# Optimization experiments

Measured on AMD Instinct MI355X. Metric: run time of the kernel, lower is better.

The kernel has to match this reference:

```python
import jax, jax.numpy as jnp
import numpy as np

# dims / config (from init_kwargs)
B, N, D, H = 8, 512, 256, 8
M, K, R = 8, 16, 8            # n_slots basis graphs, slot_dim, kernel_rank
DH = D // H
SCALE = 1.0 / float(np.sqrt(D))
TAU_AFF, TAU_SLOT = 1.0, 1.0
GW_EPS, GW_SIGMA = 0.05, 1.0
GW_OUTER, GW_SINK, TOL = 3, 10, 1e-6
G_DIV_LAMBDA, USAGE_LAMBDA, EPS = 0.1, 0.01, 1e-8


def setup_inputs() -> dict:
    key = jax.random.key(0)
    ks = jax.random.split(key, 9)
    xav = lambda k, shp: jax.random.normal(k, shp, jnp.float32) * float(np.sqrt(2.0 / (shp[-2] + shp[-1])))
    return {
        "x_desc": jax.random.normal(ks[0], (B, N, D), jnp.float32),
        "x_name": jax.random.normal(ks[1], (B, N, D), jnp.float32),
        "W1": xav(ks[2], (2 * D, D)), "b1": jnp.zeros((D,), jnp.float32),
        "W2": xav(ks[3], (D, D)),     "b2": jnp.zeros((D,), jnp.float32),
        "Wp": xav(ks[4], (D, M)),     "bp": jnp.zeros((M,), jnp.float32),
        "U_param": xav(ks[5], (M, K, R)),
    }


def _forward(x_desc, x_name, W1, b1, W2, b2, Wp, bp, U_param):
    # fusion MLP: Linear -> ReLU -> Linear
    z = jnp.concatenate([x_desc, x_name], axis=-1)          # [B,N,2D]
    z = jax.nn.relu(z @ W1 + b1) @ W2 + b2                  # [B,N,D]

    # per-head l2-normalized affinity, no self loop
    zh = z.reshape(B, N, H, DH).transpose(0, 2, 1, 3)       # [B,H,N,DH]
    zh = zh / jnp.clip(jnp.linalg.norm(zh, axis=-1, keepdims=True), 1e-8)
    logits = jnp.einsum('bhnd,bhsd->bhns', zh, zh) * (SCALE / TAU_AFF)
    logits = jnp.where(jnp.eye(N, dtype=bool), -1e9, logits)
    P = jax.nn.softmax(logits, axis=-1)                     # [B,H,N,N]

    # normalize_affinity (symmetrize + row-stochastic) -> distance
    Pn = 0.5 * (P + P.swapaxes(-1, -2))
    Pn = jnp.clip(Pn, EPS)
    Pn = Pn / jnp.clip(Pn.sum(-1, keepdims=True), EPS)
    DP = jnp.clip(1.0 - Pn, 0.0)                            # [B,H,N,N]

    # slot graphs G = softplus(U) softplus(U)^T, row-stochastic (kernel_row_stoch)
    U = jax.nn.softplus(U_param)                            # [M,K,R]
    G = jnp.einsum('mkr,mjr->mkj', U, U)                    # [M,K,K]
    G = G / jnp.clip(G.sum(-1, keepdims=True), EPS)

    # Frobenius diversity reg across the M graphs
    V = G.reshape(M, -1)
    V = V / jnp.clip(jnp.linalg.norm(V, axis=1, keepdims=True), 1e-8)
    Gram = V @ V.T
    g_reg = G_DIV_LAMBDA * (Gram.sum() - jnp.trace(Gram)) / (M * (M - 1))

    # cosine slot cost -> DG [M,K,K], zero diagonal
    diag = jnp.clip(jnp.diagonal(G, axis1=-2, axis2=-1), EPS)      # [M,K]
    denom = jnp.clip(jnp.sqrt(diag[:, :, None] * diag[:, None, :]), EPS)
    DG = jnp.clip(1.0 - jnp.clip(G / denom, -1.0, 1.0), 0.0)
    DG = DG * (1.0 - jnp.eye(K, dtype=DG.dtype))

    # entropic Gromov-Wasserstein between DP (nodes) and each DG_m (slots),
    # vectorized over the M graphs. a uniform over N, b uniform over K.
    Dx2, Dy2 = DP ** 2, DG ** 2
    a_w, b_w = 1.0 / N, 1.0 / K
    Pi = jnp.full((B, H, M, N, K), a_w * b_w, jnp.float32)

    def sinkhorn(C):
        Kmat = jnp.clip(jnp.exp(-C / GW_EPS), 1e-12)
        def body(i, uv):
            u, v = uv
            u = a_w / (jnp.einsum('bhmnk,bhmk->bhmn', Kmat, v) + TOL)
            v = b_w / (jnp.einsum('bhmnk,bhmn->bhmk', Kmat, u) + TOL)
            return (u, v)
        u0 = jnp.full((B, H, M, N), 1.0 / N, jnp.float32)
        v0 = jnp.full((B, H, M, K), 1.0 / K, jnp.float32)
        u, v = jax.lax.fori_loop(0, GW_SINK, body, (u0, v0))
        return u[..., :, None] * Kmat * v[..., None, :]

    C = None
    for _ in range(GW_OUTER):
        mass_j = Pi.sum(-1)                                  # [B,H,M,N]
        mass_l = Pi.sum(-2)                                  # [B,H,M,K]
        term1 = jnp.einsum('bhij,bhmj->bhmi', Dx2, mass_j)[..., :, None]
        term2 = jnp.einsum('mkl,bhml->bhmk', Dy2, mass_l)[..., None, :]
        cross = jnp.einsum('bhij,bhmjl,mkl->bhmik', DP, Pi, DG)
        C = jnp.clip(term1 + term2 - 2.0 * cross, 0.0)       # [B,H,M,N,K]
        Pi = sinkhorn(C)
    gw_val = (C * Pi).sum((-2, -1))                          # [B,H,M]

    # alpha weights over M graphs (alpha_from_gw)
    scores = jnp.exp(-(gw_val / GW_SIGMA) ** 2)
    alpha = scores / jnp.clip(scores.sum(-1, keepdims=True), 1e-8)

    # transport slot graphs back to node space, alpha-mix, row-normalize
    T = jnp.einsum('bhmnk,mkl->bhmnl', Pi, G)                # [B,H,M,N,K]
    Qmix = jnp.einsum('bhm,bhmnl,bhmsl->bhns', alpha, T, Pi)
    Qmix = jnp.clip(Qmix, EPS)
    Q = Qmix / Qmix.sum(-1, keepdims=True)                   # [B,H,N,N]
    bias_log = jnp.log(jax.lax.stop_gradient(Q))             # detached log-prior

    # slot usage regularizer (KL to uniform over M)
    A = jax.nn.softmax((z @ Wp + bp) / TAU_SLOT, axis=-1)     # [B,N,M]
    usage = A.mean((0, 1))
    usage_kl = jnp.sum(usage * jnp.log(jnp.clip(usage, EPS) * M))
    total_reg = g_reg + USAGE_LAMBDA * usage_kl
    return bias_log, Q, total_reg


def reference(x_desc, x_name, W1, b1, W2, b2, Wp, bp, U_param):
    return _forward(x_desc, x_name, W1, b1, W2, b2, Wp, bp, U_param)
```

## Files before the change

kernel.cpp:

```cpp
#include <hip/hip_runtime.h>
#include <cstdint>
#include <cstddef>

#define NB 8
#define NN 512
#define ND 256
#define NH 8
#define NM 8
#define NK 16
#define NR 8
#define NDH 32
#define BN (NB*NN)
#define BH (NB*NH)
#define BHN (BH*NN)
#define BHM (BH*NM)
#define QOFF 16777216

typedef __attribute__((ext_vector_type(8))) short bf16x8;
typedef __attribute__((ext_vector_type(8))) unsigned short u16x8;
typedef __attribute__((ext_vector_type(4))) float f32x4;

__device__ inline unsigned short f2bf(float x) {
  union { float f; unsigned u; } c; c.f = x;
  unsigned r = c.u + 0x7FFFu + ((c.u >> 16) & 1u);
  return (unsigned short)(r >> 16);
}
__device__ inline float bf2f(unsigned short x) {
  union { unsigned u; float f; } c; c.u = ((unsigned)x) << 16; return c.f;
}

__global__ __launch_bounds__(256) void k_mlp1(const float* __restrict__ xd, const float* __restrict__ xn,
                       const float* __restrict__ W1, const float* __restrict__ b1,
                       float* __restrict__ hid) {
  __shared__ float As[16][68];
  __shared__ float Bs[16][68];
  int t = threadIdx.x;
  int col0 = blockIdx.x * 64;
  int row0 = blockIdx.y * 64;
  int ar = t >> 2, ak = (t & 3) * 4;
  int bk = t >> 4, bc = (t & 15) * 4;
  int ty = t >> 4, tx = t & 15;
  float acc[4][4] = {};
  for (int k0 = 0; k0 < 2*ND; k0 += 16) {
    int gk = k0 + ak;
    const float* src = (gk < ND) ? (xd + (size_t)(row0+ar)*ND + gk)
                                 : (xn + (size_t)(row0+ar)*ND + (gk-ND));
    float4 av = *(const float4*)src;
    As[ak+0][ar] = av.x; As[ak+1][ar] = av.y; As[ak+2][ar] = av.z; As[ak+3][ar] = av.w;
    float4 bv = *(const float4*)(W1 + (size_t)(k0+bk)*ND + col0 + bc);
    *(float4*)&Bs[bk][bc] = bv;
    __syncthreads();
    #pragma unroll
    for (int kk = 0; kk < 16; kk++) {
      float4 a = *(const float4*)&As[kk][ty*4];
      float4 b = *(const float4*)&Bs[kk][tx*4];
      acc[0][0] += a.x*b.x; acc[0][1] += a.x*b.y; acc[0][2] += a.x*b.z; acc[0][3] += a.x*b.w;
      acc[1][0] += a.y*b.x; acc[1][1] += a.y*b.y; acc[1][2] += a.y*b.z; acc[1][3] += a.y*b.w;
      acc[2][0] += a.z*b.x; acc[2][1] += a.z*b.y; acc[2][2] += a.z*b.z; acc[2][3] += a.z*b.w;
      acc[3][0] += a.w*b.x; acc[3][1] += a.w*b.y; acc[3][2] += a.w*b.z; acc[3][3] += a.w*b.w;
    }
    __syncthreads();
  }
  float4 bb = *(const float4*)(b1 + col0 + tx*4);
  #pragma unroll
  for (int a = 0; a < 4; a++) {
    float4 o;
    o.x = fmaxf(acc[a][0] + bb.x, 0.f);
    o.y = fmaxf(acc[a][1] + bb.y, 0.f);
    o.z = fmaxf(acc[a][2] + bb.z, 0.f);
    o.w = fmaxf(acc[a][3] + bb.w, 0.f);
    *(float4*)(hid + (size_t)(row0+ty*4+a)*ND + col0 + tx*4) = o;
  }
}

__global__ __launch_bounds__(256) void k_mlp2(const float* __restrict__ hidp,
                       const float* __restrict__ W2, const float* __restrict__ b2,
                       float* __restrict__ z) {
  __shared__ float As[16][68];
  __shared__ float Bs[16][68];
  int t = threadIdx.x;
  int col0 = blockIdx.x * 64;
  int row0 = blockIdx.y * 64;
  int ar = t >> 2, ak = (t & 3) * 4;
  int bk = t >> 4, bc = (t & 15) * 4;
  int ty = t >> 4, tx = t & 15;
  float acc[4][4] = {};
  for (int k0 = 0; k0 < ND; k0 += 16) {
    float4 av = *(const float4*)(hidp + (size_t)(row0+ar)*ND + k0 + ak);
    As[ak+0][ar] = av.x; As[ak+1][ar] = av.y; As[ak+2][ar] = av.z; As[ak+3][ar] = av.w;
    float4 bv = *(const float4*)(W2 + (size_t)(k0+bk)*ND + col0 + bc);
    *(float4*)&Bs[bk][bc] = bv;
    __syncthreads();
    #pragma unroll
    for (int kk = 0; kk < 16; kk++) {
      float4 a = *(const float4*)&As[kk][ty*4];
      float4 b = *(const float4*)&Bs[kk][tx*4];
      acc[0][0] += a.x*b.x; acc[0][1] += a.x*b.y; acc[0][2] += a.x*b.z; acc[0][3] += a.x*b.w;
      acc[1][0] += a.y*b.x; acc[1][1] += a.y*b.y; acc[1][2] += a.y*b.z; acc[1][3] += a.y*b.w;
      acc[2][0] += a.z*b.x; acc[2][1] += a.z*b.y; acc[2][2] += a.z*b.z; acc[2][3] += a.z*b.w;
      acc[3][0] += a.w*b.x; acc[3][1] += a.w*b.y; acc[3][2] += a.w*b.z; acc[3][3] += a.w*b.w;
    }
    __syncthreads();
  }
  float4 bb = *(const float4*)(b2 + col0 + tx*4);
  #pragma unroll
  for (int a = 0; a < 4; a++) {
    float4 o;
    o.x = acc[a][0] + bb.x; o.y = acc[a][1] + bb.y;
    o.z = acc[a][2] + bb.z; o.w = acc[a][3] + bb.w;
    *(float4*)(z + (size_t)(row0+ty*4+a)*ND + col0 + tx*4) = o;
  }
}

__global__ void k_zhnorm(const float* __restrict__ z, float* __restrict__ zh) {
  int idx = blockIdx.x*256 + threadIdx.x;
  int d = idx & 31;
  int n = (idx >> 5) & (NN-1);
  int h = (idx >> 14) & (NH-1);
  int b = idx >> 17;
  float v = z[(size_t)(b*NN + n)*ND + h*NDH + d];
  float ss = v*v;
  #pragma unroll
  for (int m = 1; m < 32; m <<= 1) ss += __shfl_xor(ss, m);
  zh[idx] = v / fmaxf(sqrtf(ss), 1e-8f);
}

__global__ __launch_bounds__(256) void k_affinity(const float* __restrict__ zh, unsigned short* __restrict__ P) {
  int blk = blockIdx.x;
  int rt = blk & 15, bh = blk >> 4;
  int r0 = rt*32;
  const float* base = zh + (size_t)bh*NN*NDH;
  __shared__ float qs[32][33];
  __shared__ float ks[32][36];
  int t = threadIdx.x;
  int sr = t >> 3, dq = (t & 7)*4;
  {
    float4 v = *(const float4*)(base + (size_t)(r0+sr)*NDH + dq);
    qs[sr][dq] = v.x; qs[sr][dq+1] = v.y; qs[sr][dq+2] = v.z; qs[sr][dq+3] = v.w;
  }
  int cr = t >> 3;
  int cq = t & 7;
  float acc[16][4];
  #pragma unroll
  for (int ti = 0; ti < 16; ti++) { acc[ti][0]=0; acc[ti][1]=0; acc[ti][2]=0; acc[ti][3]=0; }
  for (int ti = 0; ti < 16; ti++) {
    int s0 = ti*32;
    __syncthreads();
    {
      float4 v = *(const float4*)(base + (size_t)(s0+sr)*NDH + dq);
      ks[dq+0][sr] = v.x; ks[dq+1][sr] = v.y; ks[dq+2][sr] = v.z; ks[dq+3][sr] = v.w;
    }
    __syncthreads();
    #pragma unroll
    for (int d = 0; d < 32; d++) {
      float qv = qs[cr][d];
      float4 kv = *(const float4*)&ks[d][cq*4];
      acc[ti][0] += qv*kv.x; acc[ti][1] += qv*kv.y;
      acc[ti][2] += qv*kv.z; acc[ti][3] += qv*kv.w;
    }
  }
  int gr = r0 + cr;
  float mx = -1e30f;
  #pragma unroll
  for (int ti = 0; ti < 16; ti++) {
    #pragma unroll
    for (int j = 0; j < 4; j++) {
      int s = ti*32 + cq*4 + j;
      float v = (s == gr) ? -1e9f : acc[ti][j]*0.0625f;
      acc[ti][j] = v;
      mx = fmaxf(mx, v);
    }
  }
  mx = fmaxf(mx, __shfl_xor(mx, 1));
  mx = fmaxf(mx, __shfl_xor(mx, 2));
  mx = fmaxf(mx, __shfl_xor(mx, 4));
  float sum = 0.f;
  #pragma unroll
  for (int ti = 0; ti < 16; ti++) {
    #pragma unroll
    for (int j = 0; j < 4; j++) { float e = expf(acc[ti][j]-mx); acc[ti][j] = e; sum += e; }
  }
  sum += __shfl_xor(sum,1); sum += __shfl_xor(sum,2); sum += __shfl_xor(sum,4);
  float inv = 1.f/sum;
  unsigned short* prow = P + ((size_t)(bh*NN) + gr)*NN;
  #pragma unroll
  for (int ti = 0; ti < 16; ti++) {
    uint2 pk;
    pk.x = (unsigned)f2bf(acc[ti][0]*inv) | ((unsigned)f2bf(acc[ti][1]*inv) << 16);
    pk.y = (unsigned)f2bf(acc[ti][2]*inv) | ((unsigned)f2bf(acc[ti][3]*inv) << 16);
    *(uint2*)(prow + ti*32 + cq*4) = pk;
  }
}

__global__ __launch_bounds__(256) void k_dp(const unsigned short* __restrict__ P,
                       unsigned short* __restrict__ DPo, unsigned short* __restrict__ DPq) {
  int blk = blockIdx.x;
  int rt = blk & 15, bh = blk >> 4;
  int r0 = rt*32;
  const unsigned short* Pb = P + (size_t)bh*NN*NN;
  __shared__ float Bs[32][33];
  int t = threadIdx.x;
  int r = t >> 3, q4 = (t & 7)*4;
  float pn[16][4];
  float rowacc = 0.f;
  for (int ti = 0; ti < 16; ti++) {
    int s0 = ti*32;
    __syncthreads();
    {
      uint2 v = *(const uint2*)(Pb + (size_t)(s0+r)*NN + r0 + q4);
      Bs[r][q4+0] = bf2f((unsigned short)(v.x & 0xFFFF));
      Bs[r][q4+1] = bf2f((unsigned short)(v.x >> 16));
      Bs[r][q4+2] = bf2f((unsigned short)(v.y & 0xFFFF));
      Bs[r][q4+3] = bf2f((unsigned short)(v.y >> 16));
    }
    uint2 av = *(const uint2*)(Pb + (size_t)(r0+r)*NN + s0 + q4);
    __syncthreads();
    float a0 = bf2f((unsigned short)(av.x & 0xFFFF));
    float a1 = bf2f((unsigned short)(av.x >> 16));
    float a2 = bf2f((unsigned short)(av.y & 0xFFFF));
    float a3 = bf2f((unsigned short)(av.y >> 16));
    float p0 = fmaxf(0.5f*(a0 + Bs[q4+0][r]), 1e-8f);
    float p1 = fmaxf(0.5f*(a1 + Bs[q4+1][r]), 1e-8f);
    float p2 = fmaxf(0.5f*(a2 + Bs[q4+2][r]), 1e-8f);
    float p3 = fmaxf(0.5f*(a3 + Bs[q4+3][r]), 1e-8f);
    pn[ti][0]=p0; pn[ti][1]=p1; pn[ti][2]=p2; pn[ti][3]=p3;
    rowacc += p0+p1+p2+p3;
  }
  rowacc += __shfl_xor(rowacc,1); rowacc += __shfl_xor(rowacc,2); rowacc += __shfl_xor(rowacc,4);
  float inv = 1.f / fmaxf(rowacc, 1e-8f);
  unsigned short* drow = DPo + ((size_t)(bh*NN) + r0 + r)*NN;
  unsigned short* qrow = DPq + ((size_t)(bh*NN) + r0 + r)*NN;
  #pragma unroll
  for (int ti = 0; ti < 16; ti++) {
    float o0 = fmaxf(1.f - pn[ti][0]*inv, 0.f);
    float o1 = fmaxf(1.f - pn[ti][1]*inv, 0.f);
    float o2 = fmaxf(1.f - pn[ti][2]*inv, 0.f);
    float o3 = fmaxf(1.f - pn[ti][3]*inv, 0.f);
    uint2 pk;
    pk.x = (unsigned)f2bf(o0) | ((unsigned)f2bf(o1) << 16);
    pk.y = (unsigned)f2bf(o2) | ((unsigned)f2bf(o3) << 16);
    *(uint2*)(drow + ti*32 + q4) = pk;
    uint2 qk;
    qk.x = (unsigned)f2bf(o0*o0) | ((unsigned)f2bf(o1*o1) << 16);
    qk.y = (unsigned)f2bf(o2*o2) | ((unsigned)f2bf(o3*o3) << 16);
    *(uint2*)(qrow + ti*32 + q4) = qk;
  }
}

__global__ void k_slots(const float* __restrict__ Up, float* __restrict__ G,
                        float* __restrict__ DG, float* __restrict__ greg) {
  __shared__ float U[NM*NK*NR];
  __shared__ float Gs[NM*NK*NK];
  __shared__ float rs[NM*NK];
  __shared__ float vn[NM];
  __shared__ float gram[NM*NM];
  int t = threadIdx.x;
  for (int i = t; i < NM*NK*NR; i += 256) {
    float x = Up[i];
    U[i] = fmaxf(x, 0.f) + log1pf(expf(-fabsf(x)));
  }
  __syncthreads();
  for (int i = t; i < NM*NK*NK; i += 256) {
    int m = i >> 8, k = (i >> 4) & 15, j = i & 15;
    float acc = 0.f;
    #pragma unroll
    for (int r = 0; r < NR; r++) acc += U[(m*NK+k)*NR + r]*U[(m*NK+j)*NR + r];
    Gs[i] = acc;
  }
  __syncthreads();
  for (int i = t; i < NM*NK; i += 256) {
    float s = 0.f;
    #pragma unroll
    for (int j = 0; j < NK; j++) s += Gs[i*NK + j];
    rs[i] = fmaxf(s, 1e-8f);
  }
  __syncthreads();
  for (int i = t; i < NM*NK*NK; i += 256) { Gs[i] /= rs[i >> 4]; G[i] = Gs[i]; }
  __syncthreads();
  for (int i = t; i < NM; i += 256) {
    float s = 0.f;
    for (int j = 0; j < NK*NK; j++) { float g = Gs[i*NK*NK + j]; s += g*g; }
    vn[i] = fmaxf(sqrtf(s), 1e-8f);
  }
  __syncthreads();
  for (int i = t; i < NM*NM; i += 256) {
    int a = i >> 3, b = i & 7;
    float s = 0.f;
    for (int j = 0; j < NK*NK; j++) s += Gs[a*NK*NK + j]*Gs[b*NK*NK + j];
    gram[i] = s / (vn[a]*vn[b]);
  }
  __syncthreads();
  if (t == 0) {
    float s = 0.f;
    for (int i = 0; i < NM*NM; i++) if ((i >> 3) != (i & 7)) s += gram[i];
    greg[0] = 0.1f * s / (float)(NM*(NM-1));
  }
  for (int i = t; i < NM*NK*NK; i += 256) {
    int m = i >> 8, k = (i >> 4) & 15, j = i & 15;
    float dk = fmaxf(Gs[m*NK*NK + k*NK + k], 1e-8f);
    float dj = fmaxf(Gs[m*NK*NK + j*NK + j], 1e-8f);
    float den = fmaxf(sqrtf(dk*dj), 1e-8f);
    float c = fminf(fmaxf(Gs[i]/den, -1.f), 1.f);
    float d = fmaxf(1.f - c, 0.f);
    if (k == j) d = 0.f;
    DG[i] = d;
  }
}

#define KSTR 513
#define PSTR 520
__global__ __launch_bounds__(512, 4) void k_gw(
    const unsigned short* __restrict__ DPb,
    const unsigned short* __restrict__ DPq,
    const float* __restrict__ Gm,
    const float* __restrict__ DGm,
    unsigned short* __restrict__ PiGs,
    unsigned short* __restrict__ Pis,
    float* __restrict__ gwv) {
  int blk = blockIdx.x;
  int xcd = blk & 7, seq = blk >> 3;
  int bh = xcd*8 + (seq >> 3);
  int m  = seq & 7;
  __shared__ float KT[16*KSTR];
  __shared__ unsigned short PiT[16*PSTR];
  __shared__ float u[512];
  __shared__ float vv[16], ml[16], t2s[16];
  __shared__ float Gs[16][17], DGs[16][17];
  __shared__ float sred[8][16];
  int t = threadIdx.x;
  int lane = t & 63, w = t >> 6;
  int il = lane & 15, q = lane >> 4;
  if (t < 256) { Gs[t>>4][t&15] = Gm[m*256 + t]; DGs[t>>4][t&15] = DGm[m*256 + t]; }
  for (int i = t; i < 16*PSTR; i += 512) PiT[i] = 0x3900;
  const unsigned short* DPbase = DPb + (size_t)bh*NN*NN;
  const unsigned short* DQbase = DPq + (size_t)bh*NN*NN;
  float creg[4][4];
  float gwp = 0.f;
  int rbase = w*64;
  __syncthreads();
  for (int it = 0; it < 3; ++it) {
    if (t < 16) {
      float s = 0.f;
      #pragma unroll
      for (int l = 0; l < 16; l++) { float d = DGs[t][l]; s += d*d*((it == 0) ? (1.f/16.f) : ml[l]); }
      t2s[t] = s;
    }
    __syncthreads();
    f32x4 aW0={0,0,0,0}, aW1={0,0,0,0}, aW2={0,0,0,0}, aW3={0,0,0,0};
    f32x4 aV0={0,0,0,0}, aV1={0,0,0,0}, aV2={0,0,0,0}, aV3={0,0,0,0};
    #pragma unroll 2
    for (int jt = 0; jt < 16; jt++) {
      bf16x8 af = *(const bf16x8*)&PiT[il*PSTR + jt*32 + q*8];
      const unsigned short* pr = DPbase + (size_t)(rbase + il)*NN + jt*32 + q*8;
      const unsigned short* qr = DQbase + (size_t)(rbase + il)*NN + jt*32 + q*8;
      bf16x8 w0 = *(const bf16x8*)(pr);
      bf16x8 w1 = *(const bf16x8*)(pr + 16*NN);
      bf16x8 w2 = *(const bf16x8*)(pr + 32*NN);
      bf16x8 w3 = *(const bf16x8*)(pr + 48*NN);
      bf16x8 v0 = *(const bf16x8*)(qr);
      bf16x8 v1 = *(const bf16x8*)(qr + 16*NN);
      bf16x8 v2 = *(const bf16x8*)(qr + 32*NN);
      bf16x8 v3 = *(const bf16x8*)(qr + 48*NN);
      aW0 = __builtin_amdgcn_mfma_f32_16x16x32_bf16(af, w0, aW0, 0, 0, 0);
      aW1 = __builtin_amdgcn_mfma_f32_16x16x32_bf16(af, w1, aW1, 0, 0, 0);
      aW2 = __builtin_amdgcn_mfma_f32_16x16x32_bf16(af, w2, aW2, 0, 0, 0);
      aW3 = __builtin_amdgcn_mfma_f32_16x16x32_bf16(af, w3, aW3, 0, 0, 0);
      aV0 = __builtin_amdgcn_mfma_f32_16x16x32_bf16(af, v0, aV0, 0, 0, 0);
      aV1 = __builtin_amdgcn_mfma_f32_16x16x32_bf16(af, v1, aV1, 0, 0, 0);
      aV2 = __builtin_amdgcn_mfma_f32_16x16x32_bf16(af, v2, aV2, 0, 0, 0);
      aV3 = __builtin_amdgcn_mfma_f32_16x16x32_bf16(af, v3, aV3, 0, 0, 0);
    }
    #pragma unroll
    for (int tt = 0; tt < 4; tt++) {
      f32x4 av = (tt==0)?aW0:((tt==1)?aW1:((tt==2)?aW2:aW3));
      f32x4 bv = (tt==0)?aV0:((tt==1)?aV1:((tt==2)?aV2:aV3));
      float tv = bv[0]+bv[1]+bv[2]+bv[3];
      tv += __shfl_xor(tv, 16); tv += __shfl_xor(tv, 32);
      float pc[16];
      #pragma unroll
      for (int k = 0; k < 16; k++) {
        pc[k] = av[0]*DGs[k][q*4+0] + av[1]*DGs[k][q*4+1]
              + av[2]*DGs[k][q*4+2] + av[3]*DGs[k][q*4+3];
      }
      #pragma unroll
      for (int k = 0; k < 16; k++) { pc[k] += __shfl_xor(pc[k], 16); pc[k] += __shfl_xor(pc[k], 32); }
      int i = rbase + tt*16 + il;
      #pragma unroll
      for (int kk = 0; kk < 4; kk++) {
        int k = q*4 + kk;
        float c = fmaxf(tv + t2s[k] - 2.f*pc[k], 0.f);
        creg[tt][kk] = c;
        KT[k*KSTR + i] = fmaxf(__expf(-20.f*c), 1e-12f);
      }
    }
    __syncthreads();
    if (t < 16) vv[t] = 1.f/16.f;
    __syncthreads();
    for (int si = 0; si < 10; si++) {
      float s = 0.f;
      #pragma unroll
      for (int k = 0; k < 16; k++) s += KT[k*KSTR + t]*vv[k];
      u[t] = (1.f/512.f)/(s + 1e-6f);
      __syncthreads();
      {
        int g = t >> 4, k = t & 15;
        float p = 0.f;
        #pragma unroll
        for (int jj = 0; jj < 16; jj++) { int j = g*16 + jj; p += KT[k*KSTR + j]*u[j]; }
        p += __shfl_xor(p, 16); p += __shfl_xor(p, 32);
        if (lane < 16) sred[w][lane] = p;
      }
      __syncthreads();
      if (t < 16) {
        float S = 0.f;
        #pragma unroll
        for (int w2 = 0; w2 < 8; w2++) S += sred[w2][t];
        vv[t] = (1.f/16.f)/(S + 1e-6f);
      }
      __syncthreads();
    }
    if (it < 2) {
      {
        int g = t >> 4, k = t & 15;
        float p = 0.f;
        #pragma unroll
        for (int jj = 0; jj < 16; jj++) { int j = g*16 + jj; p += KT[k*KSTR + j]*u[j]; }
        p += __shfl_xor(p, 16); p += __shfl_xor(p, 32);
        if (lane < 16) sred[w][lane] = p;
      }
      __syncthreads();
      if (t < 16) {
        float S = 0.f;
        #pragma unroll
        for (int w2 = 0; w2 < 8; w2++) S += sred[w2][t];
        ml[t] = vv[t]*S;
      }
      {
        int g = t >> 4, k = t & 15;
        float vk = vv[k];
        #pragma unroll
        for (int qq = 0; qq < 8; qq++) {
          int j0 = g*16 + qq*2;
          float p0 = u[j0]*KT[k*KSTR + j0]*vk;
          float p1 = u[j0+1]*KT[k*KSTR + j0+1]*vk;
          unsigned pk = (unsigned)f2bf(p0) | ((unsigned)f2bf(p1) << 16);
          *(unsigned*)&PiT[k*PSTR + j0] = pk;
        }
      }
      __syncthreads();
    } else {
      float pi[16];
      #pragma unroll
      for (int k = 0; k < 16; k++) pi[k] = u[t]*KT[k*KSTR + t]*vv[k];
      size_t ob = ((size_t)bh*NN + t)*128 + m*16;
      {
        uint4 w0, w1;
        w0.x = (unsigned)f2bf(pi[0])  | ((unsigned)f2bf(pi[1])  << 16);
        w0.y = (unsigned)f2bf(pi[2])  | ((unsigned)f2bf(pi[3])  << 16);
        w0.z = (unsigned)f2bf(pi[4])  | ((unsigned)f2bf(pi[5])  << 16);
        w0.w = (unsigned)f2bf(pi[6])  | ((unsigned)f2bf(pi[7])  << 16);
        w1.x = (unsigned)f2bf(pi[8])  | ((unsigned)f2bf(pi[9])  << 16);
        w1.y = (unsigned)f2bf(pi[10]) | ((unsigned)f2bf(pi[11]) << 16);
        w1.z = (unsigned)f2bf(pi[12]) | ((unsigned)f2bf(pi[13]) << 16);
        w1.w = (unsigned)f2bf(pi[14]) | ((unsigned)f2bf(pi[15]) << 16);
        *(uint4*)(Pis + ob) = w0;
        *(uint4*)(Pis + ob + 8) = w1;
      }
      float pig[16];
      #pragma unroll
      for (int l = 0; l < 16; l++) {
        float s = 0.f;
        #pragma unroll
        for (int k = 0; k < 16; k++) s += pi[k]*Gs[k][l];
        pig[l] = s;
      }
      {
        uint4 w0, w1;
        w0.x = (unsigned)f2bf(pig[0])  | ((unsigned)f2bf(pig[1])  << 16);
        w0.y = (unsigned)f2bf(pig[2])  | ((unsigned)f2bf(pig[3])  << 16);
        w0.z = (unsigned)f2bf(pig[4])  | ((unsigned)f2bf(pig[5])  << 16);
        w0.w = (unsigned)f2bf(pig[6])  | ((unsigned)f2bf(pig[7])  << 16);
        w1.x = (unsigned)f2bf(pig[8])  | ((unsigned)f2bf(pig[9])  << 16);
        w1.y = (unsigned)f2bf(pig[10]) | ((unsigned)f2bf(pig[11]) << 16);
        w1.z = (unsigned)f2bf(pig[12]) | ((unsigned)f2bf(pig[13]) << 16);
        w1.w = (unsigned)f2bf(pig[14]) | ((unsigned)f2bf(pig[15]) << 16);
        *(uint4*)(PiGs + ob) = w0;
        *(uint4*)(PiGs + ob + 8) = w1;
      }
      #pragma unroll
      for (int tt = 0; tt < 4; tt++) {
        int i = rbase + tt*16 + il;
        #pragma unroll
        for (int kk = 0; kk < 4; kk++) {
          int k = q*4 + kk;
          gwp += creg[tt][kk]*(u[i]*KT[k*KSTR + i]*vv[k]);
        }
      }
      #pragma unroll
      for (int off = 1; off < 64; off <<= 1) gwp += __shfl_xor(gwp, off);
      if (lane == 0) sred[w][0] = gwp;
      __syncthreads();
      if (t == 0) {
        float S = 0.f;
        #pragma unroll
        for (int w2 = 0; w2 < 8; w2++) S += sred[w2][0];
        gwv[bh*8 + m] = S;
      }
    }
  }
}

__global__ void k_alpha(const float* __restrict__ gw, float* __restrict__ alpha) {
  int t = threadIdx.x;
  float g = gw[t];
  float sc = expf(-(g*g));
  float s = sc;
  s += __shfl_xor(s, 1); s += __shfl_xor(s, 2); s += __shfl_xor(s, 4);
  alpha[t] = sc / fmaxf(s, 1e-8f);
}

__global__ __launch_bounds__(256) void k_qgemm(const unsigned short* __restrict__ PiGs,
                       const unsigned short* __restrict__ Pis, const float* __restrict__ alpha,
                       float* __restrict__ out) {
  int bid = blockIdx.x;
  int blk = (bid & 7)*128 + (bid >> 3);
  int strip = blk & 15, bh = blk >> 4;
  int i0 = strip*32;
  __shared__ unsigned short As[32*128];
  __shared__ unsigned short Bs[128*128];
  __shared__ float rsum[4][32];
  __shared__ float als[8];
  int t = threadIdx.x;
  int w = t >> 6, lane = t & 63;
  if (t < 8) als[t] = alpha[bh*8 + t];
  __syncthreads();
  const unsigned short* Ab = PiGs + ((size_t)bh*NN + i0)*128;
  #pragma unroll
  for (int q = 0; q < 2; q++) {
    int idx = q*256 + t;
    int r = idx >> 4, sg = idx & 15;
    float4 v = *(const float4*)(Ab + r*128 + sg*8);
    u16x8 hv = *(u16x8*)&v;
    float a = als[sg >> 1];
    u16x8 o;
    #pragma unroll
    for (int e = 0; e < 8; e++) o[e] = f2bf(bf2f(hv[e])*a);
    *(u16x8*)&As[r*128 + (sg ^ (r & 7))*8] = o;
  }
  f32x4 acc[4][2][2] = {};
  const unsigned short* Bb = Pis + (size_t)bh*NN*128;
  for (int c = 0; c < 4; c++) {
    __syncthreads();
    #pragma unroll
    for (int q = 0; q < 8; q++) {
      int idx = q*256 + t;
      int r = idx >> 4, sg = idx & 15;
      float4 v = *(const float4*)(Bb + (size_t)(c*128 + r)*128 + sg*8);
      *(float4*)&Bs[r*128 + (sg ^ (r & 7))*8] = v;
    }
    __syncthreads();
    int col0 = w*32;
    #pragma unroll
    for (int ks = 0; ks < 4; ks++) {
      int slot = (ks*4 + (lane >> 4)) ^ (lane & 7);
      int la = lane & 15;
      bf16x8 a0 = *(bf16x8*)&As[la*128 + slot*8];
      bf16x8 a1 = *(bf16x8*)&As[(la+16)*128 + slot*8];
      bf16x8 b0 = *(bf16x8*)&Bs[(col0+la)*128 + slot*8];
      bf16x8 b1 = *(bf16x8*)&Bs[(col0+la+16)*128 + slot*8];
      acc[c][0][0] = __builtin_amdgcn_mfma_f32_16x16x32_bf16(a0, b0, acc[c][0][0], 0, 0, 0);
      acc[c][1][0] = __builtin_amdgcn_mfma_f32_16x16x32_bf16(a1, b0, acc[c][1][0], 0, 0, 0);
      acc[c][0][1] = __builtin_amdgcn_mfma_f32_16x16x32_bf16(a0, b1, acc[c][0][1], 0, 0, 0);
      acc[c][1][1] = __builtin_amdgcn_mfma_f32_16x16x32_bf16(a1, b1, acc[c][1][1], 0, 0, 0);
    }
  }
  float part[2][4];
  #pragma unroll
  for (int mt = 0; mt < 2; mt++) {
    #pragma unroll
    for (int rg = 0; rg < 4; rg++) {
      float s = 0.f;
      #pragma unroll
      for (int c = 0; c < 4; c++) {
        #pragma unroll
        for (int nt = 0; nt < 2; nt++) s += fmaxf(acc[c][mt][nt][rg], 1e-8f);
      }
      s += __shfl_xor(s, 1); s += __shfl_xor(s, 2);
      s += __shfl_xor(s, 4); s += __shfl_xor(s, 8);
      part[mt][rg] = s;
    }
  }
  if ((lane & 15) == 0) {
    int rgrp = lane >> 4;
    #pragma unroll
    for (int mt = 0; mt < 2; mt++)
      #pragma unroll
      for (int rg = 0; rg < 4; rg++)
        rsum[w][mt*16 + rgrp*4 + rg] = part[mt][rg];
  }
  __syncthreads();
  float invr[2][4];
  #pragma unroll
  for (int mt = 0; mt < 2; mt++) {
    #pragma unroll
    for (int rg = 0; rg < 4; rg++) {
      int row = mt*16 + (lane >> 4)*4 + rg;
      invr[mt][rg] = 1.f / (rsum[0][row] + rsum[1][row] + rsum[2][row] + rsum[3][row]);
    }
  }
  float* Qb = out + (size_t)QOFF + ((size_t)bh*NN + i0)*NN;
  float* Lb = out + ((size_t)bh*NN + i0)*NN;
  #pragma unroll
  for (int c = 0; c < 4; c++) {
    #pragma unroll
    for (int mt = 0; mt < 2; mt++) {
      #pragma unroll
      for (int nt = 0; nt < 2; nt++) {
        #pragma unroll
        for (int rg = 0; rg < 4; rg++) {
          int row = mt*16 + (lane >> 4)*4 + rg;
          int col = c*128 + w*32 + nt*16 + (lane & 15);
          float v = fmaxf(acc[c][mt][nt][rg], 1e-8f)*invr[mt][rg];
          Qb[(size_t)row*NN + col] = v;
          Lb[(size_t)row*NN + col] = __logf(v);
        }
      }
    }
  }
}

__global__ __launch_bounds__(256) void k_usage(const float* __restrict__ z, const float* __restrict__ Wp,
                        const float* __restrict__ bp, float* __restrict__ partial) {
  __shared__ float wps[256][9];
  __shared__ float red[256][8];
  int t = threadIdx.x;
  {
    float4 a = *(const float4*)(Wp + t*8);
    float4 b = *(const float4*)(Wp + t*8 + 4);
    wps[t][0]=a.x; wps[t][1]=a.y; wps[t][2]=a.z; wps[t][3]=a.w;
    wps[t][4]=b.x; wps[t][5]=b.y; wps[t][6]=b.z; wps[t][7]=b.w;
  }
  __syncthreads();
  int row = blockIdx.x*256 + t;
  const float* zr = z + (size_t)row*ND;
  float acc[8] = {};
  for (int d0 = 0; d0 < ND; d0 += 4) {
    float4 v = *(const float4*)(zr + d0);
    #pragma unroll
    for (int m = 0; m < 8; m++) {
      acc[m] += v.x*wps[d0][m] + v.y*wps[d0+1][m] + v.z*wps[d0+2][m] + v.w*wps[d0+3][m];
    }
  }
  float mx = -1e30f;
  #pragma unroll
  for (int m = 0; m < 8; m++) { acc[m] += bp[m]; mx = fmaxf(mx, acc[m]); }
  float s = 0.f;
  #pragma unroll
  for (int m = 0; m < 8; m++) { acc[m] = expf(acc[m]-mx); s += acc[m]; }
  float inv = 1.f/s;
  #pragma unroll
  for (int m = 0; m < 8; m++) red[t][m] = acc[m]*inv;
  __syncthreads();
  for (int q = 128; q > 0; q >>= 1) {
    if (t < q) { for (int m = 0; m < 8; m++) red[t][m] += red[t+q][m]; }
    __syncthreads();
  }
  if (t < 8) partial[blockIdx.x*8 + t] = red[0][t];
}

__global__ void k_final(const float* __restrict__ greg, const float* __restrict__ partial,
                        float* __restrict__ out) {
  if (threadIdx.x == 0) {
    float us[8] = {};
    for (int b = 0; b < 16; b++)
      for (int m = 0; m < 8; m++) us[m] += partial[b*8 + m];
    float kl = 0.f;
    for (int m = 0; m < 8; m++) {
      float u = us[m] / (float)BN;
      kl += u*logf(fmaxf(u, 1e-8f)*(float)NM);
    }
    out[33554432] = greg[0] + 0.01f*kl;
  }
}

extern "C" void kernel_launch(void* const* d_in, const int* in_sizes, int n_in,
                              void* d_out, int out_size, void* d_ws, size_t ws_size,
                              hipStream_t stream) {
  const float* xd = (const float*)d_in[0];
  const float* xn = (const float*)d_in[1];
  const float* W1 = (const float*)d_in[2];
  const float* b1 = (const float*)d_in[3];
  const float* W2 = (const float*)d_in[4];
  const float* b2 = (const float*)d_in[5];
  const float* Wp = (const float*)d_in[6];
  const float* bp = (const float*)d_in[7];
  const float* Up = (const float*)d_in[8];
  float* out = (float*)d_out;
  float* ws  = (float*)d_ws;

  float* z   = ws + 0;
  float* hid = ws + 1048576;
  float* zh  = ws + 2097152;
  unsigned short* PiGs = (unsigned short*)(ws + 3145728);
  unsigned short* Pis  = (unsigned short*)(ws + 5242880);
  float* gw    = ws + 7340032;
  float* alpha = ws + 7340544;
  float* G     = ws + 7341056;
  float* DG    = ws + 7343104;
  float* greg  = ws + 7345152;
  float* partial = ws + 7345153;

  unsigned short* P16 = (unsigned short*)out;
  unsigned short* DPb = (unsigned short*)(out + QOFF);
  unsigned short* DPq = DPb + (size_t)16777216;

  k_mlp1<<<dim3(4, 64), 256, 0, stream>>>(xd, xn, W1, b1, hid);
  k_mlp2<<<dim3(4, 64), 256, 0, stream>>>(hid, W2, b2, z);
  k_usage<<<16, 256, 0, stream>>>(z, Wp, bp, partial);
  k_zhnorm<<<4096, 256, 0, stream>>>(z, zh);
  k_affinity<<<1024, 256, 0, stream>>>(zh, P16);
  k_dp<<<1024, 256, 0, stream>>>(P16, DPb, DPq);
  k_slots<<<1, 256, 0, stream>>>(Up, G, DG, greg);
  k_gw<<<512, 512, 0, stream>>>(DPb, DPq, G, DG, PiGs, Pis, gw);
  k_alpha<<<1, 512, 0, stream>>>(gw, alpha);
  k_qgemm<<<1024, 256, 0, stream>>>(PiGs, Pis, alpha, out);
  k_final<<<1, 64, 0, stream>>>(greg, partial, out);
}
```

Measured before the change: 590.1 us.

## Skip first GW cost GEMM via row sums; stage DP tiles in LDS; bf16 kernel

Row sums of DP and DP² are now produced in the DP kernel, so the first outer GW iteration, where Pi is uniform, builds the cost matrix from those sums and skips the two DP GEMMs entirely. The remaining iterations stream DP and DP² tiles through a register-prefetched LDS buffer instead of each wave reading global memory directly. The Gibbs kernel is stored in LDS as bf16 and also kept in registers. Sinkhorn marginals are folded into the last inner iteration to drop an extra reduction. This cuts global traffic and GEMM work, at the cost of more block barriers, more LDS use per block, and bf16 rounding of the kernel matrix.

```diff
diff --git a/kernel.cpp b/kernel.cpp
--- a/kernel.cpp
+++ b/kernel.cpp
@@ -27,6 +27,12 @@
 }
 __device__ inline float bf2f(unsigned short x) {
   union { unsigned u; float f; } c; c.u = ((unsigned)x) << 16; return c.f;
+}
+__device__ inline float bflo(unsigned w2) {
+  union { unsigned u; float f; } c; c.u = w2 << 16; return c.f;
+}
+__device__ inline float bfhi(unsigned w2) {
+  union { unsigned u; float f; } c; c.u = w2 & 0xFFFF0000u; return c.f;
 }
 
 __global__ __launch_bounds__(256) void k_mlp1(const float* __restrict__ xd, const float* __restrict__ xn,
@@ -193,7 +199,8 @@
 }
 
 __global__ __launch_bounds__(256) void k_dp(const unsigned short* __restrict__ P,
-                       unsigned short* __restrict__ DPo, unsigned short* __restrict__ DPq) {
+                       unsigned short* __restrict__ DPo, unsigned short* __restrict__ DPq,
+                       float* __restrict__ rs, float* __restrict__ rq) {
   int blk = blockIdx.x;
   int rt = blk & 15, bh = blk >> 4;
   int r0 = rt*32;
@@ -230,12 +237,15 @@
   float inv = 1.f / fmaxf(rowacc, 1e-8f);
   unsigned short* drow = DPo + ((size_t)(bh*NN) + r0 + r)*NN;
   unsigned short* qrow = DPq + ((size_t)(bh*NN) + r0 + r)*NN;
+  float rsv = 0.f, rqv = 0.f;
   #pragma unroll
   for (int ti = 0; ti < 16; ti++) {
     float o0 = fmaxf(1.f - pn[ti][0]*inv, 0.f);
     float o1 = fmaxf(1.f - pn[ti][1]*inv, 0.f);
     float o2 = fmaxf(1.f - pn[ti][2]*inv, 0.f);
     float o3 = fmaxf(1.f - pn[ti][3]*inv, 0.f);
+    rsv += o0+o1+o2+o3;
+    rqv += o0*o0 + o1*o1 + o2*o2 + o3*o3;
     uint2 pk;
     pk.x = (unsigned)f2bf(o0) | ((unsigned)f2bf(o1) << 16);
     pk.y = (unsigned)f2bf(o2) | ((unsigned)f2bf(o3) << 16);
@@ -245,13 +255,19 @@
     qk.y = (unsigned)f2bf(o2*o2) | ((unsigned)f2bf(o3*o3) << 16);
     *(uint2*)(qrow + ti*32 + q4) = qk;
   }
+  rsv += __shfl_xor(rsv,1); rsv += __shfl_xor(rsv,2); rsv += __shfl_xor(rsv,4);
+  rqv += __shfl_xor(rqv,1); rqv += __shfl_xor(rqv,2); rqv += __shfl_xor(rqv,4);
+  if ((t & 7) == 0) {
+    rs[bh*NN + r0 + r] = rsv;
+    rq[bh*NN + r0 + r] = rqv;
+  }
 }
 
 __global__ void k_slots(const float* __restrict__ Up, float* __restrict__ G,
                         float* __restrict__ DG, float* __restrict__ greg) {
   __shared__ float U[NM*NK*NR];
   __shared__ float Gs[NM*NK*NK];
-  __shared__ float rs[NM*NK];
+  __shared__ float rsx[NM*NK];
   __shared__ float vn[NM];
   __shared__ float gram[NM*NM];
   int t = threadIdx.x;
@@ -272,10 +288,10 @@
     float s = 0.f;
     #pragma unroll
     for (int j = 0; j < NK; j++) s += Gs[i*NK + j];
-    rs[i] = fmaxf(s, 1e-8f);
-  }
-  __syncthreads();
-  for (int i = t; i < NM*NK*NK; i += 256) { Gs[i] /= rs[i >> 4]; G[i] = Gs[i]; }
+    rsx[i] = fmaxf(s, 1e-8f);
+  }
+  __syncthreads();
+  for (int i = t; i < NM*NK*NK; i += 256) { Gs[i] /= rsx[i >> 4]; G[i] = Gs[i]; }
   __syncthreads();
   for (int i = t; i < NM; i += 256) {
     float s = 0.f;
@@ -307,151 +323,213 @@
   }
 }
 
-#define KSTR 513
+#define DSTR 40
+#define KST 522
 #define PSTR 520
 __global__ __launch_bounds__(512, 4) void k_gw(
     const unsigned short* __restrict__ DPb,
     const unsigned short* __restrict__ DPq,
-    const float* __restrict__ Gm,
-    const float* __restrict__ DGm,
-    unsigned short* __restrict__ PiGs,
-    unsigned short* __restrict__ Pis,
+    const float* __restrict__ rs, const float* __restrict__ rq,
+    const float* __restrict__ Gm, const float* __restrict__ DGm,
+    unsigned short* __restrict__ PiGs, unsigned short* __restrict__ Pis,
     float* __restrict__ gwv) {
   int blk = blockIdx.x;
   int xcd = blk & 7, seq = blk >> 3;
   int bh = xcd*8 + (seq >> 3);
   int m  = seq & 7;
-  __shared__ float KT[16*KSTR];
-  __shared__ unsigned short PiT[16*PSTR];
-  __shared__ float u[512];
-  __shared__ float vv[16], ml[16], t2s[16];
-  __shared__ float Gs[16][17], DGs[16][17];
+  __shared__ __align__(16) unsigned short DPs[512*DSTR];
+  __shared__ __align__(16) unsigned short KT[16*KST];
+  __shared__ __align__(16) unsigned short PiT[16*PSTR];
+  __shared__ __align__(16) float u[512];
+  __shared__ __align__(16) float vv[16];
+  __shared__ float ml[16], t2s[16], dgrow[16];
+  __shared__ float Gsm[16][17], DGsm[16][17];
   __shared__ float sred[8][16];
   int t = threadIdx.x;
   int lane = t & 63, w = t >> 6;
   int il = lane & 15, q = lane >> 4;
-  if (t < 256) { Gs[t>>4][t&15] = Gm[m*256 + t]; DGs[t>>4][t&15] = DGm[m*256 + t]; }
-  for (int i = t; i < 16*PSTR; i += 512) PiT[i] = 0x3900;
+  int g = t >> 4, kc = t & 15;
+  if (t < 256) { Gsm[t>>4][t&15] = Gm[m*256 + t]; DGsm[t>>4][t&15] = DGm[m*256 + t]; }
+  __syncthreads();
+  if (t < 16) {
+    float s = 0.f;
+    #pragma unroll
+    for (int l = 0; l < 16; l++) s += DGsm[t][l];
+    dgrow[t] = s;
+  }
   const unsigned short* DPbase = DPb + (size_t)bh*NN*NN;
   const unsigned short* DQbase = DPq + (size_t)bh*NN*NN;
+  float rsv = rs[bh*NN + t]*(1.f/8192.f);
+  float rqv = rq[bh*NN + t]*(1.f/512.f);
+  float Kt[16];
   float creg[4][4];
-  float gwp = 0.f;
-  int rbase = w*64;
-  __syncthreads();
-  for (int it = 0; it < 3; ++it) {
+  float ut = 0.f;
+  int r0i = t >> 2, ci = (t & 3)*8;
+  for (int itr = 0; itr < 3; ++itr) {
     if (t < 16) {
       float s = 0.f;
       #pragma unroll
-      for (int l = 0; l < 16; l++) { float d = DGs[t][l]; s += d*d*((it == 0) ? (1.f/16.f) : ml[l]); }
+      for (int l = 0; l < 16; l++) { float d = DGsm[t][l]; s += d*d*((itr == 0) ? (1.f/16.f) : ml[l]); }
       t2s[t] = s;
     }
     __syncthreads();
-    f32x4 aW0={0,0,0,0}, aW1={0,0,0,0}, aW2={0,0,0,0}, aW3={0,0,0,0};
-    f32x4 aV0={0,0,0,0}, aV1={0,0,0,0}, aV2={0,0,0,0}, aV3={0,0,0,0};
-    #pragma unroll 2
-    for (int jt = 0; jt < 16; jt++) {
-      bf16x8 af = *(const bf16x8*)&PiT[il*PSTR + jt*32 + q*8];
-      const unsigned short* pr = DPbase + (size_t)(rbase + il)*NN + jt*32 + q*8;
-      const unsigned short* qr = DQbase + (size_t)(rbase + il)*NN + jt*32 + q*8;
-      bf16x8 w0 = *(const bf16x8*)(pr);
-      bf16x8 w1 = *(const bf16x8*)(pr + 16*NN);
-      bf16x8 w2 = *(const bf16x8*)(pr + 32*NN);
-      bf16x8 w3 = *(const bf16x8*)(pr + 48*NN);
-      bf16x8 v0 = *(const bf16x8*)(qr);
-      bf16x8 v1 = *(const bf16x8*)(qr + 16*NN);
-      bf16x8 v2 = *(const bf16x8*)(qr + 32*NN);
-      bf16x8 v3 = *(const bf16x8*)(qr + 48*NN);
-      aW0 = __builtin_amdgcn_mfma_f32_16x16x32_bf16(af, w0, aW0, 0, 0, 0);
-      aW1 = __builtin_amdgcn_mfma_f32_16x16x32_bf16(af, w1, aW1, 0, 0, 0);
-      aW2 = __builtin_amdgcn_mfma_f32_16x16x32_bf16(af, w2, aW2, 0, 0, 0);
-      aW3 = __builtin_amdgcn_mfma_f32_16x16x32_bf16(af, w3, aW3, 0, 0, 0);
-      aV0 = __builtin_amdgcn_mfma_f32_16x16x32_bf16(af, v0, aV0, 0, 0, 0);
-      aV1 = __builtin_amdgcn_mfma_f32_16x16x32_bf16(af, v1, aV1, 0, 0, 0);
-      aV2 = __builtin_amdgcn_mfma_f32_16x16x32_bf16(af, v2, aV2, 0, 0, 0);
-      aV3 = __builtin_amdgcn_mfma_f32_16x16x32_bf16(af, v3, aV3, 0, 0, 0);
-    }
-    #pragma unroll
-    for (int tt = 0; tt < 4; tt++) {
-      f32x4 av = (tt==0)?aW0:((tt==1)?aW1:((tt==2)?aW2:aW3));
-      f32x4 bv = (tt==0)?aV0:((tt==1)?aV1:((tt==2)?aV2:aV3));
-      float tv = bv[0]+bv[1]+bv[2]+bv[3];
-      tv += __shfl_xor(tv, 16); tv += __shfl_xor(tv, 32);
-      float pc[16];
+    if (itr == 0) {
       #pragma unroll
       for (int k = 0; k < 16; k++) {
-        pc[k] = av[0]*DGs[k][q*4+0] + av[1]*DGs[k][q*4+1]
-              + av[2]*DGs[k][q*4+2] + av[3]*DGs[k][q*4+3];
-      }
-      #pragma unroll
-      for (int k = 0; k < 16; k++) { pc[k] += __shfl_xor(pc[k], 16); pc[k] += __shfl_xor(pc[k], 32); }
-      int i = rbase + tt*16 + il;
-      #pragma unroll
-      for (int kk = 0; kk < 4; kk++) {
-        int k = q*4 + kk;
-        float c = fmaxf(tv + t2s[k] - 2.f*pc[k], 0.f);
-        creg[tt][kk] = c;
-        KT[k*KSTR + i] = fmaxf(__expf(-20.f*c), 1e-12f);
-      }
+        float c = fmaxf(rqv + t2s[k] - 2.f*rsv*dgrow[k], 0.f);
+        float e = fmaxf(__expf(-20.f*c), 1e-12f);
+        Kt[k] = e;
+        KT[k*KST + t] = f2bf(e);
+      }
+    } else {
+      f32x4 aW0={0,0,0,0}, aW1={0,0,0,0}, aW2={0,0,0,0}, aW3={0,0,0,0};
+      f32x4 aV0={0,0,0,0}, aV1={0,0,0,0}, aV2={0,0,0,0}, aV3={0,0,0,0};
+      float4 c0, c1, c2, c3;
+      c0 = *(const float4*)(DPbase + (size_t)r0i*NN + ci);
+      c1 = *(const float4*)(DPbase + (size_t)(r0i+128)*NN + ci);
+      c2 = *(const float4*)(DPbase + (size_t)(r0i+256)*NN + ci);
+      c3 = *(const float4*)(DPbase + (size_t)(r0i+384)*NN + ci);
+      for (int p = 0; p < 16; p++) {
+        *(float4*)&DPs[r0i*DSTR + ci] = c0;
+        *(float4*)&DPs[(r0i+128)*DSTR + ci] = c1;
+        *(float4*)&DPs[(r0i+256)*DSTR + ci] = c2;
+        *(float4*)&DPs[(r0i+384)*DSTR + ci] = c3;
+        __syncthreads();
+        {
+          const unsigned short* src = (p < 15) ? (DPbase + (p+1)*32) : DQbase;
+          c0 = *(const float4*)(src + (size_t)r0i*NN + ci);
+          c1 = *(const float4*)(src + (size_t)(r0i+128)*NN + ci);
+          c2 = *(const float4*)(src + (size_t)(r0i+256)*NN + ci);
+          c3 = *(const float4*)(src + (size_t)(r0i+384)*NN + ci);
+        }
+        bf16x8 af = *(const bf16x8*)&PiT[il*PSTR + p*32 + q*8];
+        bf16x8 b0 = *(const bf16x8*)&DPs[(w*64 + il)*DSTR + q*8];
+        bf16x8 b1 = *(const bf16x8*)&DPs[(w*64 + 16 + il)*DSTR + q*8];
+        bf16x8 b2 = *(const bf16x8*)&DPs[(w*64 + 32 + il)*DSTR + q*8];
+        bf16x8 b3 = *(const bf16x8*)&DPs[(w*64 + 48 + il)*DSTR + q*8];
+        aW0 = __builtin_amdgcn_mfma_f32_16x16x32_bf16(af, b0, aW0, 0, 0, 0);
+        aW1 = __builtin_amdgcn_mfma_f32_16x16x32_bf16(af, b1, aW1, 0, 0, 0);
+        aW2 = __builtin_amdgcn_mfma_f32_16x16x32_bf16(af, b2, aW2, 0, 0, 0);
+        aW3 = __builtin_amdgcn_mfma_f32_16x16x32_bf16(af, b3, aW3, 0, 0, 0);
+        __syncthreads();
+      }
+      for (int p = 0; p < 16; p++) {
+        *(float4*)&DPs[r0i*DSTR + ci] = c0;
+        *(float4*)&DPs[(r0i+128)*DSTR + ci] = c1;
+        *(float4*)&DPs[(r0i+256)*DSTR + ci] = c2;
+        *(float4*)&DPs[(r0i+384)*DSTR + ci] = c3;
+        __syncthreads();
+        if (p < 15) {
+          const unsigned short* src = DQbase + (p+1)*32;
+          c0 = *(const float4*)(src + (size_t)r0i*NN + ci);
+          c1 = *(const float4*)(src + (size_t)(r0i+128)*NN + ci);
+          c2 = *(const float4*)(src + (size_t)(r0i+256)*NN + ci);
+          c3 = *(const float4*)(src + (size_t)(r0i+384)*NN + ci);
+        }
+        bf16x8 af = *(const bf16x8*)&PiT[il*PSTR + p*32 + q*8];
+        bf16x8 b0 = *(const bf16x8*)&DPs[(w*64 + il)*DSTR + q*8];
+        bf16x8 b1 = *(const bf16x8*)&DPs[(w*64 + 16 + il)*DSTR + q*8];
+        bf16x8 b2 = *(const bf16x8*)&DPs[(w*64 + 32 + il)*DSTR + q*8];
+        bf16x8 b3 = *(const bf16x8*)&DPs[(w*64 + 48 + il)*DSTR + q*8];
+        aV0 = __builtin_amdgcn_mfma_f32_16x16x32_bf16(af, b0, aV0, 0, 0, 0);
+        aV1 = __builtin_amdgcn_mfma_f32_16x16x32_bf16(af, b1, aV1, 0, 0, 0);
+        aV2 = __builtin_amdgcn_mfma_f32_16x16x32_bf16(af, b2, aV2, 0, 0, 0);
+        aV3 = __builtin_amdgcn_mfma_f32_16x16x32_bf16(af, b3, aV3, 0, 0, 0);
+        __syncthreads();
+      }
+      #pragma unroll
+      for (int tt = 0; tt < 4; tt++) {
+        f32x4 av = (tt==0)?aW0:((tt==1)?aW1:((tt==2)?aW2:aW3));
+        f32x4 bv = (tt==0)?aV0:((tt==1)?aV1:((tt==2)?aV2:aV3));
+        float tv = bv[0]+bv[1]+bv[2]+bv[3];
+        tv += __shfl_xor(tv, 16); tv += __shfl_xor(tv, 32);
+        float pc[16];
+        #pragma unroll
+        for (int k = 0; k < 16; k++) {
+          pc[k] = av[0]*DGsm[k][q*4+0] + av[1]*DGsm[k][q*4+1]
+                + av[2]*DGsm[k][q*4+2] + av[3]*DGsm[k][q*4+3];
+        }
+        #pragma unroll
+        for (int k = 0; k < 16; k++) { pc[k] += __shfl_xor(pc[k], 16); pc[k] += __shfl_xor(pc[k], 32); }
+        int i = w*64 + tt*16 + il;
+        #pragma unroll
+        for (int kk = 0; kk < 4; kk++) {
+          int k = q*4 + kk;
+          float c = fmaxf(tv + t2s[k] - 2.f*pc[k], 0.f);
+          creg[tt][kk] = c;
+          KT[k*KST + i] = f2bf(fmaxf(__expf(-20.f*c), 1e-12f));
+        }
+      }
+      __syncthreads();
+      #pragma unroll
+      for (int k = 0; k < 16; k++) Kt[k] = bf2f(KT[k*KST + t]);
     }
     __syncthreads();
     if (t < 16) vv[t] = 1.f/16.f;
     __syncthreads();
     for (int si = 0; si < 10; si++) {
-      float s = 0.f;
-      #pragma unroll
-      for (int k = 0; k < 16; k++) s += KT[k*KSTR + t]*vv[k];
-      u[t] = (1.f/512.f)/(s + 1e-6f);
+      float4 va = *(const float4*)&vv[0];
+      float4 vb = *(const float4*)&vv[4];
+      float4 vc = *(const float4*)&vv[8];
+      float4 vd = *(const float4*)&vv[12];
+      float s = Kt[0]*va.x + Kt[1]*va.y + Kt[2]*va.z + Kt[3]*va.w
+              + Kt[4]*vb.x + Kt[5]*vb.y + Kt[6]*vb.z + Kt[7]*vb.w
+              + Kt[8]*vc.x + Kt[9]*vc.y + Kt[10]*vc.z + Kt[11]*vc.w
+              + Kt[12]*vd.x + Kt[13]*vd.y + Kt[14]*vd.z + Kt[15]*vd.w;
+      ut = (1.f/512.f)/(s + 1e-6f);
+      u[t] = ut;
       __syncthreads();
-      {
-        int g = t >> 4, k = t & 15;
-        float p = 0.f;
-        #pragma unroll
-        for (int jj = 0; jj < 16; jj++) { int j = g*16 + jj; p += KT[k*KSTR + j]*u[j]; }
-        p += __shfl_xor(p, 16); p += __shfl_xor(p, 32);
-        if (lane < 16) sred[w][lane] = p;
-      }
+      const unsigned* kp = (const unsigned*)&KT[kc*KST + g*16];
+      unsigned k0 = kp[0], k1 = kp[1], k2 = kp[2], k3 = kp[3];
+      unsigned k4 = kp[4], k5 = kp[5], k6 = kp[6], k7 = kp[7];
+      float4 ua = *(const float4*)&u[g*16];
+      float4 ub = *(const float4*)&u[g*16+4];
+      float4 uc = *(const float4*)&u[g*16+8];
+      float4 ud = *(const float4*)&u[g*16+12];
+      float p = bflo(k0)*ua.x + bfhi(k0)*ua.y + bflo(k1)*ua.z + bfhi(k1)*ua.w
+              + bflo(k2)*ub.x + bfhi(k2)*ub.y + bflo(k3)*ub.z + bfhi(k3)*ub.w
+              + bflo(k4)*uc.x + bfhi(k4)*uc.y + bflo(k5)*uc.z + bfhi(k5)*uc.w
+              + bflo(k6)*ud.x + bfhi(k6)*ud.y + bflo(k7)*ud.z + bfhi(k7)*ud.w;
+      p += __shfl_xor(p, 16); p += __shfl_xor(p, 32);
+      if (lane < 16) sred[w][lane] = p;
       __syncthreads();
       if (t < 16) {
-        float S = 0.f;
-        #pragma unroll
-        for (int w2 = 0; w2 < 8; w2++) S += sred[w2][t];
-        vv[t] = (1.f/16.f)/(S + 1e-6f);
+        float S = sred[0][t]+sred[1][t]+sred[2][t]+sred[3][t]
+                + sred[4][t]+sred[5][t]+sred[6][t]+sred[7][t];
+        float nv = (1.f/16.f)/(S + 1e-6f);
+        vv[t] = nv;
+        ml[t] = nv*S;
       }
       __syncthreads();
     }
-    if (it < 2) {
-      {
-        int g = t >> 4, k = t & 15;
-        float p = 0.f;
-        #pragma unroll
-        for (int jj = 0; jj < 16; jj++) { int j = g*16 + jj; p += KT[k*KSTR + j]*u[j]; }
-        p += __shfl_xor(p, 16); p += __shfl_xor(p, 32);
-        if (lane < 16) sred[w][lane] = p;
-      }
-      __syncthreads();
-      if (t < 16) {
-        float S = 0.f;
-        #pragma unroll
-        for (int w2 = 0; w2 < 8; w2++) S += sred[w2][t];
-        ml[t] = vv[t]*S;
-      }
-      {
-        int g = t >> 4, k = t & 15;
-        float vk = vv[k];
-        #pragma unroll
-        for (int qq = 0; qq < 8; qq++) {
-          int j0 = g*16 + qq*2;
-          float p0 = u[j0]*KT[k*KSTR + j0]*vk;
-          float p1 = u[j0+1]*KT[k*KSTR + j0+1]*vk;
-          unsigned pk = (unsigned)f2bf(p0) | ((unsigned)f2bf(p1) << 16);
-          *(unsigned*)&PiT[k*PSTR + j0] = pk;
-        }
-      }
+    if (itr < 2) {
+      const unsigned* kp = (const unsigned*)&KT[kc*KST + g*16];
+      float4 ua = *(const float4*)&u[g*16];
+      float4 ub = *(const float4*)&u[g*16+4];
+      float4 uc = *(const float4*)&u[g*16+8];
+      float4 ud = *(const float4*)&u[g*16+12];
+      float vk = vv[kc];
+      unsigned* pp = (unsigned*)&PiT[kc*PSTR + g*16];
+      unsigned kx;
+      kx = kp[0]; pp[0] = (unsigned)f2bf(ua.x*bflo(kx)*vk) | ((unsigned)f2bf(ua.y*bfhi(kx)*vk) << 16);
+      kx = kp[1]; pp[1] = (unsigned)f2bf(ua.z*bflo(kx)*vk) | ((unsigned)f2bf(ua.w*bfhi(kx)*vk) << 16);
+      kx = kp[2]; pp[2] = (unsigned)f2bf(ub.x*bflo(kx)*vk) | ((unsigned)f2bf(ub.y*bfhi(kx)*vk) << 16);
+      kx = kp[3]; pp[3] = (unsigned)f2bf(ub.z*bflo(kx)*vk) | ((unsigned)f2bf(ub.w*bfhi(kx)*vk) << 16);
+      kx = kp[4]; pp[4] = (unsigned)f2bf(uc.x*bflo(kx)*vk) | ((unsigned)f2bf(uc.y*bfhi(kx)*vk) << 16);
+      kx = kp[5]; pp[5] = (unsigned)f2bf(uc.z*bflo(kx)*vk) | ((unsigned)f2bf(uc.w*bfhi(kx)*vk) << 16);
+      kx = kp[6]; pp[6] = (unsigned)f2bf(ud.x*bflo(kx)*vk) | ((unsigned)f2bf(ud.y*bfhi(kx)*vk) << 16);
+      kx = kp[7]; pp[7] = (unsigned)f2bf(ud.z*bflo(kx)*vk) | ((unsigned)f2bf(ud.w*bfhi(kx)*vk) << 16);
       __syncthreads();
     } else {
+      float4 va = *(const float4*)&vv[0];
+      float4 vb = *(const float4*)&vv[4];
+      float4 vc = *(const float4*)&vv[8];
+      float4 vd = *(const float4*)&vv[12];
+      float vr[16] = {va.x,va.y,va.z,va.w, vb.x,vb.y,vb.z,vb.w,
+                      vc.x,vc.y,vc.z,vc.w, vd.x,vd.y,vd.z,vd.w};
       float pi[16];
       #pragma unroll
-      for (int k = 0; k < 16; k++) pi[k] = u[t]*KT[k*KSTR + t]*vv[k];
+      for (int k = 0; k < 16; k++) pi[k] = ut*Kt[k]*vr[k];
       size_t ob = ((size_t)bh*NN + t)*128 + m*16;
       {
         uint4 w0, w1;
@@ -471,7 +549,7 @@
       for (int l = 0; l < 16; l++) {
         float s = 0.f;
         #pragma unroll
-        for (int k = 0; k < 16; k++) s += pi[k]*Gs[k][l];
+        for (int k = 0; k < 16; k++) s += pi[k]*Gsm[k][l];
         pig[l] = s;
       }
       {
@@ -487,13 +565,15 @@
         *(uint4*)(PiGs + ob) = w0;
         *(uint4*)(PiGs + ob + 8) = w1;
       }
+      float gwp = 0.f;
       #pragma unroll
       for (int tt = 0; tt < 4; tt++) {
-        int i = rbase + tt*16 + il;
+        int i = w*64 + tt*16 + il;
+        float ui = u[i];
         #pragma unroll
         for (int kk = 0; kk < 4; kk++) {
           int k = q*4 + kk;
-          gwp += creg[tt][kk]*(u[i]*KT[k*KSTR + i]*vv[k]);
+          gwp += creg[tt][kk]*(ui*bf2f(KT[k*KST + i])*vr[k]);
         }
       }
       #pragma unroll
@@ -512,8 +592,8 @@
 
 __global__ void k_alpha(const float* __restrict__ gw, float* __restrict__ alpha) {
   int t = threadIdx.x;
-  float g = gw[t];
-  float sc = expf(-(g*g));
+  float gg = gw[t];
+  float sc = expf(-(gg*gg));
   float s = sc;
   s += __shfl_xor(s, 1); s += __shfl_xor(s, 2); s += __shfl_xor(s, 4);
   alpha[t] = sc / fmaxf(s, 1e-8f);
@@ -709,6 +789,8 @@
   float* DG    = ws + 7343104;
   float* greg  = ws + 7345152;
   float* partial = ws + 7345153;
+  float* rsb   = ws + 7345664;
+  float* rqb   = ws + 7378432;
 
   unsigned short* P16 = (unsigned short*)out;
   unsigned short* DPb = (unsigned short*)(out + QOFF);
@@ -719,9 +801,9 @@
   k_usage<<<16, 256, 0, stream>>>(z, Wp, bp, partial);
   k_zhnorm<<<4096, 256, 0, stream>>>(z, zh);
   k_affinity<<<1024, 256, 0, stream>>>(zh, P16);
-  k_dp<<<1024, 256, 0, stream>>>(P16, DPb, DPq);
+  k_dp<<<1024, 256, 0, stream>>>(P16, DPb, DPq, rsb, rqb);
   k_slots<<<1, 256, 0, stream>>>(Up, G, DG, greg);
-  k_gw<<<512, 512, 0, stream>>>(DPb, DPq, G, DG, PiGs, Pis, gw);
+  k_gw<<<512, 512, 0, stream>>>(DPb, DPq, rsb, rqb, G, DG, PiGs, Pis, gw);
   k_alpha<<<1, 512, 0, stream>>>(gw, alpha);
   k_qgemm<<<1024, 256, 0, stream>>>(PiGs, Pis, alpha, out);
   k_final<<<1, 64, 0, stream>>>(greg, partial, out);
```

Result: faster. 519.4 us (-12.0%).
